# Performance work log

Measured on AMD Instinct MI355X. Metric: run time of the kernel, lower is better.

The kernel has to match this reference:

```python
import jax, jax.numpy as jnp
import numpy as np

B, S, D = 2, 2048, 1024
H, DH, DM = 16, 64, 4096
EPS = 1e-5
IGNORE = -100000.0


def setup_inputs() -> dict:
    key = jax.random.key(0)
    ks = jax.random.split(key, 14)
    s = 0.02
    return {
        "x": jax.random.normal(ks[0], (B, S, D), jnp.float32),
        "W_Q": jax.random.normal(ks[1], (H, DH, D), jnp.float32) * s,
        "W_K": jax.random.normal(ks[2], (H, DH, D), jnp.float32) * s,
        "W_V": jax.random.normal(ks[3], (H, DH, D), jnp.float32) * s,
        "W_O": jax.random.normal(ks[4], (H, D, DH), jnp.float32) * s,
        "b_Q": jax.random.normal(ks[5], (H, DH), jnp.float32) * s,
        "b_K": jax.random.normal(ks[6], (H, DH), jnp.float32) * s,
        "b_V": jax.random.normal(ks[7], (H, DH), jnp.float32) * s,
        "b_O": jax.random.normal(ks[8], (D,), jnp.float32) * s,
        "W_in": jax.random.normal(ks[9], (DM, D), jnp.float32) * s,
        "b_in": jax.random.normal(ks[10], (DM,), jnp.float32) * s,
        "W_out": jax.random.normal(ks[11], (D, DM), jnp.float32) * s,
        "b_out": jax.random.normal(ks[12], (D,), jnp.float32) * s,
    }


def ln_pre(x):
    x = x - jnp.mean(x, axis=-1, keepdims=True)
    scale = jnp.sqrt(jnp.mean(x * x, axis=-1, keepdims=True) + EPS)
    return x / scale


def gelu_new(x):
    c = np.sqrt(2.0 / np.pi).astype(np.float32)
    return 0.5 * x * (1.0 + jnp.tanh(c * (x + 0.044715 * x ** 3)))


def reference(x, W_Q, W_K, W_V, W_O, b_Q, b_K, b_V, b_O, W_in, b_in, W_out, b_out):
    resid_pre = x
    xn = ln_pre(resid_pre)
    # q,k,v: [B, S, H, DH]
    q = jnp.einsum('ihm,bpm->bpih', W_Q, xn) + b_Q
    k = jnp.einsum('ihm,bpm->bpih', W_K, xn) + b_K
    v = jnp.einsum('ihm,bpm->bpih', W_V, xn) + b_V
    attn_scale = np.sqrt(DH).astype(np.float32)
    # scores: [B, H, Sq, Sk]  (einsum 'bpih,bqih->bipq')
    scores = jnp.einsum('bpih,bqih->bipq', q, k) / attn_scale
    mask = jnp.tril(jnp.ones((S, S), bool))
    scores = jnp.where(mask, scores, IGNORE)
    attn = jax.nn.softmax(scores, axis=-1)
    # z: [B, Sq, H, DH]
    z = jnp.einsum('bpih,biqp->bqih', v, attn)
    attn_out = jnp.einsum('idh,bqih->bqd', W_O, z) + b_O
    resid_mid = resid_pre + attn_out
    m = ln_pre(resid_mid)
    pre = jnp.einsum('md,bpd->bpm', W_in, m) + b_in
    post = gelu_new(pre)
    mlp_out = jnp.einsum('dm,bpm->bpd', W_out, post) + b_out
    return resid_mid + mlp_out
```

## Files before the change

### kernel.cpp

```cpp
#include <hip/hip_runtime.h>

typedef unsigned short u16;
typedef __attribute__((ext_vector_type(8))) short short8;
typedef __attribute__((ext_vector_type(4))) unsigned short ushort4v;
typedef __attribute__((ext_vector_type(4))) float float4v;

__device__ __forceinline__ float bf2f(u16 u) {
  union { unsigned int i; float f; } c; c.i = ((unsigned int)u) << 16; return c.f;
}
__device__ __forceinline__ u16 f2bf(float f) {
  union { float f; unsigned int i; } c; c.f = f;
  unsigned int u = c.i;
  return (u16)((u + 0x7fffu + ((u >> 16) & 1u)) >> 16);
}
__device__ __forceinline__ float gelu_new(float x) {
  const float k1 = 2.30218776f;
  const float k3 = 0.10294233f;
  float x3 = x * x * x;
  float e = __builtin_amdgcn_exp2f(-(k1 * x + k3 * x3));
  return x / (1.0f + e);
}
__device__ __forceinline__ float ldres(const float* p) { return *p; }
__device__ __forceinline__ float ldres(const u16* p) { return bf2f(*p); }

__device__ __forceinline__ void gload_lds16(const u16* g, u16* l) {
  __builtin_amdgcn_global_load_lds(
      (const __attribute__((address_space(1))) unsigned int*)g,
      (__attribute__((address_space(3))) unsigned int*)l, 16, 0, 0);
}

__global__ void cvt_bf16(const float* __restrict__ src, u16* __restrict__ dst) {
  int t = blockIdx.x * 256 + threadIdx.x;
  float4v a = *(const float4v*)(src + (size_t)t * 8);
  float4v b = *(const float4v*)(src + (size_t)t * 8 + 4);
  short8 o;
#pragma unroll
  for (int j = 0; j < 4; ++j) o[j] = (short)f2bf(a[j]);
#pragma unroll
  for (int j = 0; j < 4; ++j) o[4 + j] = (short)f2bf(b[j]);
  *(short8*)(dst + (size_t)t * 8) = o;
}

__global__ void prep_wo(const float* __restrict__ WO, u16* __restrict__ Wot) {
  int t = blockIdx.x * 256 + threadIdx.x;
  int i = t >> 13;
  int d = (t >> 3) & 1023;
  int h0 = (t & 7) * 8;
  const float* src = WO + (size_t)i * 65536 + d * 64 + h0;
  float4v a = *(const float4v*)(src);
  float4v b = *(const float4v*)(src + 4);
  short8 o;
#pragma unroll
  for (int j = 0; j < 4; ++j) o[j] = (short)f2bf(a[j]);
#pragma unroll
  for (int j = 0; j < 4; ++j) o[4 + j] = (short)f2bf(b[j]);
  *(short8*)(Wot + (size_t)d * 1024 + i * 64 + h0) = o;
}

__global__ void prep_bqkv(const float* __restrict__ bQ, const float* __restrict__ bK,
                          const float* __restrict__ bV, float* __restrict__ bqkv) {
  int t = blockIdx.x * 256 + threadIdx.x;
  if (t < 3072)
    bqkv[t] = (t < 1024) ? bQ[t] : (t < 2048) ? bK[t - 1024] : bV[t - 2048];
}

__global__ void ln_f32(const float* __restrict__ x, u16* __restrict__ y) {
  __shared__ float red1[4];
  __shared__ float red2[4];
  int token = blockIdx.x;
  int tid = threadIdx.x;
  int w = tid >> 6;
  const float* xr = x + (size_t)token * 1024;
  float4v v = *(const float4v*)(xr + tid * 4);
  float s = v[0] + v[1] + v[2] + v[3];
#pragma unroll
  for (int m = 32; m >= 1; m >>= 1) s += __shfl_xor(s, m);
  if ((tid & 63) == 0) red1[w] = s;
  __syncthreads();
  float mean = (red1[0] + red1[1] + red1[2] + red1[3]) * (1.0f / 1024.0f);
  float ss = 0.0f;
#pragma unroll
  for (int j = 0; j < 4; ++j) { v[j] -= mean; ss += v[j] * v[j]; }
#pragma unroll
  for (int m = 32; m >= 1; m >>= 1) ss += __shfl_xor(ss, m);
  if ((tid & 63) == 0) red2[w] = ss;
  __syncthreads();
  float ms = (red2[0] + red2[1] + red2[2] + red2[3]) * (1.0f / 1024.0f);
  float inv = 1.0f / sqrtf(ms + 1e-5f);
  ushort4v o;
#pragma unroll
  for (int j = 0; j < 4; ++j) o[j] = f2bf(v[j] * inv);
  *(ushort4v*)(y + (size_t)token * 1024 + tid * 4) = o;
}

template <int BN, int BK, bool GELU, bool VSPLIT, typename TO, typename TR>
__global__ __launch_bounds__(256) void gemm_bt(
    const u16* __restrict__ A, const u16* __restrict__ Bw,
    const float* __restrict__ bias, const TR* __restrict__ resid,
    TO* __restrict__ C, u16* __restrict__ vTout, int M, int N, int K,
    int lda, int ldc) {
  constexpr int BM = 128;
  constexpr int SEGS = BK / 8;
  constexpr int FI = 4, FJ = BN / 32;
  constexpr int CA = BM * SEGS / 256;
  constexpr int CB = BN * SEGS / 256;
  __shared__ __align__(16) u16 As[BM * BK];
  __shared__ __align__(16) u16 Bs[BN * BK];
  const int tid = threadIdx.x;
  const int w = tid >> 6, lane = tid & 63;
  const int quad = lane >> 4, l16 = lane & 15;
  const int m0 = blockIdx.x * BM, n0 = blockIdx.y * BN;
  const int wm = (w >> 1) * 64, wn = (w & 1) * (BN / 2);
  float4v acc[FI][FJ] = {};
  for (int k0 = 0; k0 < K; k0 += BK) {
    __syncthreads();
#pragma unroll
    for (int t = 0; t < CA; ++t) {
      int chunk = (w * CA + t) * 64 + lane;
      int row = chunk / SEGS, seg = chunk % SEGS;
      gload_lds16(A + (size_t)(m0 + row) * lda + k0 + seg * 8,
                  As + (w * CA + t) * 512);
    }
#pragma unroll
    for (int t = 0; t < CB; ++t) {
      int chunk = (w * CB + t) * 64 + lane;
      int row = chunk / SEGS, seg = chunk % SEGS;
      gload_lds16(Bw + (size_t)(n0 + row) * K + k0 + seg * 8,
                  Bs + (w * CB + t) * 512);
    }
    __syncthreads();
#pragma unroll
    for (int kk = 0; kk < BK; kk += 32) {
      short8 a[FI], b[FJ];
#pragma unroll
      for (int fi = 0; fi < FI; ++fi)
        a[fi] = *(const short8*)(As + (wm + fi * 16 + l16) * BK + kk + quad * 8);
#pragma unroll
      for (int fj = 0; fj < FJ; ++fj)
        b[fj] = *(const short8*)(Bs + (wn + fj * 16 + l16) * BK + kk + quad * 8);
#pragma unroll
      for (int fi = 0; fi < FI; ++fi)
#pragma unroll
        for (int fj = 0; fj < FJ; ++fj)
          acc[fi][fj] = __builtin_amdgcn_mfma_f32_16x16x32_bf16(
              a[fi], b[fj], acc[fi][fj], 0, 0, 0);
    }
  }
#pragma unroll
  for (int fi = 0; fi < FI; ++fi) {
#pragma unroll
    for (int fj = 0; fj < FJ; ++fj) {
      int col = n0 + wn + fj * 16 + l16;
      float bv = bias ? bias[col] : 0.0f;
#pragma unroll
      for (int r = 0; r < 4; ++r) {
        int row = m0 + wm + fi * 16 + quad * 4 + r;
        float val = acc[fi][fj][r] + bv;
        if (resid) val += ldres(resid + (size_t)row * N + col);
        if (GELU) val = gelu_new(val);
        if (VSPLIT && col >= 2048) {
          vTout[(size_t)(col - 2048) * 4096 + row] = f2bf(val);
        } else if constexpr (sizeof(TO) == 2) {
          C[(size_t)row * ldc + col] = f2bf(val);
        } else {
          C[(size_t)row * ldc + col] = val;
        }
      }
    }
  }
}

__global__ __launch_bounds__(256) void attn_flash(u16* __restrict__ qk,
                                                  const u16* __restrict__ vT) {
  constexpr int PADK = 72;
  constexpr float C2 = 0.18033688011112042f;
  __shared__ __align__(16) u16 Ks[64 * PADK];
  __shared__ __align__(16) u16 Vt[64 * PADK];
  __shared__ __align__(16) u16 Ps[4][16 * PADK];
  const int id = blockIdx.x;
  const int qt = 31 - (id >> 5);
  const int combo = id & 31;
  const int head = combo >> 1, b = combo & 1;
  const int tid = threadIdx.x;
  const int w = tid >> 6, lane = tid & 63;
  const int quad = lane >> 4, l16 = lane & 15;
  const int q0 = qt * 64;
  const size_t tokB = (size_t)b * 2048;

  short8 aq[2];
#pragma unroll
  for (int ks = 0; ks < 2; ++ks)
    aq[ks] = *(const short8*)(qk + (tokB + q0 + w * 16 + l16) * 2048 +
                              head * 64 + ks * 32 + quad * 8);

  const u16* kbase = qk + tokB * 2048 + 1024 + head * 64;
  const u16* vbase = vT + (size_t)head * 64 * 4096 + tokB;

  float m_st[4] = {-1e30f, -1e30f, -1e30f, -1e30f};
  float l_st[4] = {0.f, 0.f, 0.f, 0.f};
  float4v o_acc[4] = {};

  for (int kt = 0; kt <= qt; ++kt) {
    const int kk0 = kt * 64;
    __syncthreads();
#pragma unroll
    for (int i = 0; i < 2; ++i) {
      int flat = tid * 2 + i;
      int row = flat >> 3, seg = flat & 7;
      *(short8*)(Ks + row * PADK + seg * 8) =
          *(const short8*)(kbase + (size_t)(kk0 + row) * 2048 + seg * 8);
      *(short8*)(Vt + row * PADK + seg * 8) =
          *(const short8*)(vbase + (size_t)row * 4096 + kk0 + seg * 8);
    }
    __syncthreads();

    float4v s[4];
#pragma unroll
    for (int fj = 0; fj < 4; ++fj) {
      float4v t = {0.f, 0.f, 0.f, 0.f};
#pragma unroll
      for (int ks = 0; ks < 2; ++ks) {
        short8 bk = *(const short8*)(Ks + (fj * 16 + l16) * PADK + ks * 32 + quad * 8);
        t = __builtin_amdgcn_mfma_f32_16x16x32_bf16(aq[ks], bk, t, 0, 0, 0);
      }
      s[fj] = t;
    }
#pragma unroll
    for (int fj = 0; fj < 4; ++fj)
#pragma unroll
      for (int r = 0; r < 4; ++r) s[fj][r] *= C2;
    if (kt == qt) {
#pragma unroll
      for (int fj = 0; fj < 4; ++fj) {
        int col = kk0 + fj * 16 + l16;
#pragma unroll
        for (int r = 0; r < 4; ++r) {
          int row = q0 + w * 16 + quad * 4 + r;
          if (col > row) s[fj][r] = -1e30f;
        }
      }
    }
    float mx[4];
#pragma unroll
    for (int r = 0; r < 4; ++r) {
      float m = s[0][r];
#pragma unroll
      for (int fj = 1; fj < 4; ++fj) m = fmaxf(m, s[fj][r]);
      m = fmaxf(m, __shfl_xor(m, 1));
      m = fmaxf(m, __shfl_xor(m, 2));
      m = fmaxf(m, __shfl_xor(m, 4));
      m = fmaxf(m, __shfl_xor(m, 8));
      mx[r] = m;
    }
    float alpha[4];
#pragma unroll
    for (int r = 0; r < 4; ++r) {
      float mnew = fmaxf(m_st[r], mx[r]);
      alpha[r] = __builtin_amdgcn_exp2f(m_st[r] - mnew);
      m_st[r] = mnew;
    }
    float rs[4] = {0.f, 0.f, 0.f, 0.f};
#pragma unroll
    for (int fj = 0; fj < 4; ++fj)
#pragma unroll
      for (int r = 0; r < 4; ++r) {
        float pv = __builtin_amdgcn_exp2f(s[fj][r] - m_st[r]);
        s[fj][r] = pv;
        rs[r] += pv;
      }
#pragma unroll
    for (int r = 0; r < 4; ++r) {
      float t = rs[r];
      t += __shfl_xor(t, 1);
      t += __shfl_xor(t, 2);
      t += __shfl_xor(t, 4);
      t += __shfl_xor(t, 8);
      l_st[r] = l_st[r] * alpha[r] + t;
    }
#pragma unroll
    for (int fj = 0; fj < 4; ++fj)
#pragma unroll
      for (int r = 0; r < 4; ++r) o_acc[fj][r] *= alpha[r];
#pragma unroll
    for (int fj = 0; fj < 4; ++fj)
#pragma unroll
      for (int r = 0; r < 4; ++r)
        Ps[w][(quad * 4 + r) * PADK + fj * 16 + l16] = f2bf(s[fj][r]);
    short8 ap[2];
#pragma unroll
    for (int ks = 0; ks < 2; ++ks)
      ap[ks] = *(const short8*)(&Ps[w][l16 * PADK + ks * 32 + quad * 8]);
#pragma unroll
    for (int fj = 0; fj < 4; ++fj)
#pragma unroll
      for (int ks = 0; ks < 2; ++ks) {
        short8 bv = *(const short8*)(Vt + (fj * 16 + l16) * PADK + ks * 32 + quad * 8);
        o_acc[fj] = __builtin_amdgcn_mfma_f32_16x16x32_bf16(ap[ks], bv, o_acc[fj], 0, 0, 0);
      }
  }
#pragma unroll
  for (int r = 0; r < 4; ++r) {
    float inv = 1.0f / l_st[r];
    int row = q0 + w * 16 + quad * 4 + r;
#pragma unroll
    for (int fj = 0; fj < 4; ++fj)
      qk[(tokB + row) * 2048 + head * 64 + fj * 16 + l16] =
          f2bf(o_acc[fj][r] * inv);
  }
}

extern "C" void kernel_launch(void* const* d_in, const int* in_sizes, int n_in,
                              void* d_out, int out_size, void* d_ws, size_t ws_size,
                              hipStream_t stream) {
  const float* x = (const float*)d_in[0];
  const float* W_Q = (const float*)d_in[1];
  const float* W_K = (const float*)d_in[2];
  const float* W_V = (const float*)d_in[3];
  const float* W_O = (const float*)d_in[4];
  const float* b_Q = (const float*)d_in[5];
  const float* b_K = (const float*)d_in[6];
  const float* b_V = (const float*)d_in[7];
  const float* b_O = (const float*)d_in[8];
  const float* W_in = (const float*)d_in[9];
  const float* b_in = (const float*)d_in[10];
  const float* W_out = (const float*)d_in[11];
  const float* b_out = (const float*)d_in[12];
  float* out = (float*)d_out;

  char* ws = (char*)d_ws;
  u16* Wqkv = (u16*)(ws);
  u16* Wot  = (u16*)(ws + 6291456);
  u16* Wib  = (u16*)(ws + 8388608);
  u16* Wob  = (u16*)(ws + 16777216);
  float* bqkv = (float*)(ws + 25165824);
  u16* xn   = (u16*)(ws + 25178112);
  u16* qk   = (u16*)(ws + 33566720);
  u16* vT   = (u16*)(ws + 50343936);
  u16* hbuf = (u16*)(ws + 33566720);
  float* rm = (float*)(ws + 67121152);

  cvt_bf16<<<512, 256, 0, stream>>>(W_Q, Wqkv);
  cvt_bf16<<<512, 256, 0, stream>>>(W_K, Wqkv + 1048576);
  cvt_bf16<<<512, 256, 0, stream>>>(W_V, Wqkv + 2097152);
  cvt_bf16<<<2048, 256, 0, stream>>>(W_in, Wib);
  cvt_bf16<<<2048, 256, 0, stream>>>(W_out, Wob);
  prep_wo<<<512, 256, 0, stream>>>(W_O, Wot);
  prep_bqkv<<<12, 256, 0, stream>>>(b_Q, b_K, b_V, bqkv);

  ln_f32<<<4096, 256, 0, stream>>>(x, xn);
  gemm_bt<128, 32, false, true, u16, float><<<dim3(32, 24), 256, 0, stream>>>(
      xn, Wqkv, bqkv, (const float*)nullptr, qk, vT, 4096, 3072, 1024, 1024, 2048);
  attn_flash<<<1024, 256, 0, stream>>>(qk, vT);
  gemm_bt<64, 64, false, false, float, float><<<dim3(32, 16), 256, 0, stream>>>(
      qk , Wot, b_O, x, rm, nullptr, 4096, 1024, 1024, 2048, 1024);
  ln_f32<<<4096, 256, 0, stream>>>(rm, xn);
  gemm_bt<128, 32, true, false, u16, float><<<dim3(32, 32), 256, 0, stream>>>(
      xn, Wib, b_in, (const float*)nullptr, hbuf, nullptr, 4096, 4096, 1024, 1024, 4096);
  gemm_bt<64, 64, false, false, float, float><<<dim3(32, 16), 256, 0, stream>>>(
      hbuf, Wob, b_out, rm, out, nullptr, 4096, 1024, 4096, 4096, 1024);
}
```

Before: 423.9 us.

## Use split-K with atomic accumulation for the W_O and W_out projections

Adds a split-K mode to the GEMM. Each z-slice computes a partial K range and atomically adds its result into a pre-zeroed fp32 output, and only slice 0 adds the bias and residual. The two N=1024 projection GEMMs switch to 128x128 tiles with 2-way and 4-way K splits. This keeps the block count up while using larger tiles. The cost is two memsets and fp32 atomic traffic, and the floating-point summation order becomes nondeterministic.

```diff
diff --git a/kernel.cpp b/kernel.cpp
--- a/kernel.cpp
+++ b/kernel.cpp
@@ -93,12 +93,12 @@
   *(ushort4v*)(y + (size_t)token * 1024 + tid * 4) = o;
 }
 
-template <int BN, int BK, bool GELU, bool VSPLIT, typename TO, typename TR>
+template <int BN, int BK, bool GELU, bool VSPLIT, bool ATOMIC, typename TO, typename TR>
 __global__ __launch_bounds__(256) void gemm_bt(
     const u16* __restrict__ A, const u16* __restrict__ Bw,
     const float* __restrict__ bias, const TR* __restrict__ resid,
     TO* __restrict__ C, u16* __restrict__ vTout, int M, int N, int K,
-    int lda, int ldc) {
+    int lda, int ldc, int kPer) {
   constexpr int BM = 128;
   constexpr int SEGS = BK / 8;
   constexpr int FI = 4, FJ = BN / 32;
@@ -111,8 +111,9 @@
   const int quad = lane >> 4, l16 = lane & 15;
   const int m0 = blockIdx.x * BM, n0 = blockIdx.y * BN;
   const int wm = (w >> 1) * 64, wn = (w & 1) * (BN / 2);
+  const int kBase = ATOMIC ? blockIdx.z * kPer : 0;
   float4v acc[FI][FJ] = {};
-  for (int k0 = 0; k0 < K; k0 += BK) {
+  for (int k0 = kBase; k0 < kBase + kPer; k0 += BK) {
     __syncthreads();
 #pragma unroll
     for (int t = 0; t < CA; ++t) {
@@ -146,19 +147,22 @@
               a[fi], b[fj], acc[fi][fj], 0, 0, 0);
     }
   }
+  const bool lead = !ATOMIC || blockIdx.z == 0;
 #pragma unroll
   for (int fi = 0; fi < FI; ++fi) {
 #pragma unroll
     for (int fj = 0; fj < FJ; ++fj) {
       int col = n0 + wn + fj * 16 + l16;
-      float bv = bias ? bias[col] : 0.0f;
+      float bv = (bias && lead) ? bias[col] : 0.0f;
 #pragma unroll
       for (int r = 0; r < 4; ++r) {
         int row = m0 + wm + fi * 16 + quad * 4 + r;
         float val = acc[fi][fj][r] + bv;
-        if (resid) val += ldres(resid + (size_t)row * N + col);
+        if (resid && lead) val += ldres(resid + (size_t)row * N + col);
         if (GELU) val = gelu_new(val);
-        if (VSPLIT && col >= 2048) {
+        if constexpr (ATOMIC) {
+          unsafeAtomicAdd((float*)(C + (size_t)row * ldc + col), val);
+        } else if (VSPLIT && col >= 2048) {
           vTout[(size_t)(col - 2048) * 4096 + row] = f2bf(val);
         } else if constexpr (sizeof(TO) == 2) {
           C[(size_t)row * ldc + col] = f2bf(val);
@@ -339,6 +343,9 @@
   u16* hbuf = (u16*)(ws + 33566720);
   float* rm = (float*)(ws + 67121152);
 
+  hipMemsetAsync(rm, 0, (size_t)4096 * 1024 * 4, stream);
+  hipMemsetAsync(out, 0, (size_t)4096 * 1024 * 4, stream);
+
   cvt_bf16<<<512, 256, 0, stream>>>(W_Q, Wqkv);
   cvt_bf16<<<512, 256, 0, stream>>>(W_K, Wqkv + 1048576);
   cvt_bf16<<<512, 256, 0, stream>>>(W_V, Wqkv + 2097152);
@@ -348,14 +355,14 @@
   prep_bqkv<<<12, 256, 0, stream>>>(b_Q, b_K, b_V, bqkv);
 
   ln_f32<<<4096, 256, 0, stream>>>(x, xn);
-  gemm_bt<128, 32, false, true, u16, float><<<dim3(32, 24), 256, 0, stream>>>(
-      xn, Wqkv, bqkv, (const float*)nullptr, qk, vT, 4096, 3072, 1024, 1024, 2048);
+  gemm_bt<128, 32, false, true, false, u16, float><<<dim3(32, 24), 256, 0, stream>>>(
+      xn, Wqkv, bqkv, (const float*)nullptr, qk, vT, 4096, 3072, 1024, 1024, 2048, 1024);
   attn_flash<<<1024, 256, 0, stream>>>(qk, vT);
-  gemm_bt<64, 64, false, false, float, float><<<dim3(32, 16), 256, 0, stream>>>(
-      qk , Wot, b_O, x, rm, nullptr, 4096, 1024, 1024, 2048, 1024);
+  gemm_bt<128, 32, false, false, true, float, float><<<dim3(32, 8, 2), 256, 0, stream>>>(
+      qk , Wot, b_O, x, rm, nullptr, 4096, 1024, 1024, 2048, 1024, 512);
   ln_f32<<<4096, 256, 0, stream>>>(rm, xn);
-  gemm_bt<128, 32, true, false, u16, float><<<dim3(32, 32), 256, 0, stream>>>(
-      xn, Wib, b_in, (const float*)nullptr, hbuf, nullptr, 4096, 4096, 1024, 1024, 4096);
-  gemm_bt<64, 64, false, false, float, float><<<dim3(32, 16), 256, 0, stream>>>(
-      hbuf, Wob, b_out, rm, out, nullptr, 4096, 1024, 4096, 4096, 1024);
-}
+  gemm_bt<128, 32, true, false, false, u16, float><<<dim3(32, 32), 256, 0, stream>>>(
+      xn, Wib, b_in, (const float*)nullptr, hbuf, nullptr, 4096, 4096, 1024, 1024, 4096, 1024);
+  gemm_bt<128, 32, false, false, true, float, float><<<dim3(32, 8, 4), 256, 0, stream>>>(
+      hbuf, Wob, b_out, rm, out, nullptr, 4096, 1024, 4096, 4096, 1024, 1024);
+}
```

New measurement: 471.1 us. 11.2% more time.

## Add XOR-swizzled LDS layout, double buffering, and larger K tiles to GEMM

Applied to the files above, without the earlier changes.

The GEMM kernel now XOR-swizzles 16-byte segments within each LDS row. Fragment reads for the MFMA then avoid bank conflicts. An optional double-buffered path is added and enabled for the two N=1024 GEMMs; it prefetches the next K tile while computing the current one, using one barrier per iteration instead of two. The QKV and MLP-in GEMMs switch from BK=32 to BK=64, which halves the loop iterations. Double buffering doubles LDS use and may reduce occupancy.

```diff
diff --git a/kernel.cpp b/kernel.cpp
--- a/kernel.cpp
+++ b/kernel.cpp
@@ -93,7 +93,7 @@
   *(ushort4v*)(y + (size_t)token * 1024 + tid * 4) = o;
 }
 
-template <int BN, int BK, bool GELU, bool VSPLIT, typename TO, typename TR>
+template <int BN, int BK, bool GELU, bool VSPLIT, bool DBUF, typename TO, typename TR>
 __global__ __launch_bounds__(256) void gemm_bt(
     const u16* __restrict__ A, const u16* __restrict__ Bw,
     const float* __restrict__ bias, const TR* __restrict__ resid,
@@ -101,43 +101,51 @@
     int lda, int ldc) {
   constexpr int BM = 128;
   constexpr int SEGS = BK / 8;
+  constexpr int SMASK = SEGS - 1;
   constexpr int FI = 4, FJ = BN / 32;
   constexpr int CA = BM * SEGS / 256;
   constexpr int CB = BN * SEGS / 256;
-  __shared__ __align__(16) u16 As[BM * BK];
-  __shared__ __align__(16) u16 Bs[BN * BK];
+  constexpr int NB = DBUF ? 2 : 1;
+  __shared__ __align__(16) u16 As[NB][BM * BK];
+  __shared__ __align__(16) u16 Bs[NB][BN * BK];
   const int tid = threadIdx.x;
   const int w = tid >> 6, lane = tid & 63;
   const int quad = lane >> 4, l16 = lane & 15;
   const int m0 = blockIdx.x * BM, n0 = blockIdx.y * BN;
   const int wm = (w >> 1) * 64, wn = (w & 1) * (BN / 2);
+  const int rmask = l16 & SMASK;
   float4v acc[FI][FJ] = {};
-  for (int k0 = 0; k0 < K; k0 += BK) {
-    __syncthreads();
+
+  auto stage = [&](int buf, int k0) {
 #pragma unroll
     for (int t = 0; t < CA; ++t) {
       int chunk = (w * CA + t) * 64 + lane;
       int row = chunk / SEGS, seg = chunk % SEGS;
-      gload_lds16(A + (size_t)(m0 + row) * lda + k0 + seg * 8,
-                  As + (w * CA + t) * 512);
+      int sseg = seg ^ (row & SMASK);
+      gload_lds16(A + (size_t)(m0 + row) * lda + k0 + sseg * 8,
+                  As[buf] + (w * CA + t) * 512);
     }
 #pragma unroll
     for (int t = 0; t < CB; ++t) {
       int chunk = (w * CB + t) * 64 + lane;
       int row = chunk / SEGS, seg = chunk % SEGS;
-      gload_lds16(Bw + (size_t)(n0 + row) * K + k0 + seg * 8,
-                  Bs + (w * CB + t) * 512);
-    }
-    __syncthreads();
+      int sseg = seg ^ (row & SMASK);
+      gload_lds16(Bw + (size_t)(n0 + row) * K + k0 + sseg * 8,
+                  Bs[buf] + (w * CB + t) * 512);
+    }
+  };
+  auto compute = [&](int buf) {
 #pragma unroll
     for (int kk = 0; kk < BK; kk += 32) {
       short8 a[FI], b[FJ];
 #pragma unroll
       for (int fi = 0; fi < FI; ++fi)
-        a[fi] = *(const short8*)(As + (wm + fi * 16 + l16) * BK + kk + quad * 8);
+        a[fi] = *(const short8*)(As[buf] + (wm + fi * 16 + l16) * BK +
+                                 ((((kk >> 3) + quad) ^ rmask) << 3));
 #pragma unroll
       for (int fj = 0; fj < FJ; ++fj)
-        b[fj] = *(const short8*)(Bs + (wn + fj * 16 + l16) * BK + kk + quad * 8);
+        b[fj] = *(const short8*)(Bs[buf] + (wn + fj * 16 + l16) * BK +
+                                 ((((kk >> 3) + quad) ^ rmask) << 3));
 #pragma unroll
       for (int fi = 0; fi < FI; ++fi)
 #pragma unroll
@@ -145,7 +153,27 @@
           acc[fi][fj] = __builtin_amdgcn_mfma_f32_16x16x32_bf16(
               a[fi], b[fj], acc[fi][fj], 0, 0, 0);
     }
+  };
+
+  if constexpr (DBUF) {
+    stage(0, 0);
+    __syncthreads();
+    int cur = 0;
+    for (int k0 = 0; k0 < K; k0 += BK) {
+      if (k0 + BK < K) stage(cur ^ 1, k0 + BK);
+      compute(cur);
+      __syncthreads();
+      cur ^= 1;
+    }
+  } else {
+    for (int k0 = 0; k0 < K; k0 += BK) {
+      __syncthreads();
+      stage(0, k0);
+      __syncthreads();
+      compute(0);
+    }
   }
+
 #pragma unroll
   for (int fi = 0; fi < FI; ++fi) {
 #pragma unroll
@@ -348,14 +376,14 @@
   prep_bqkv<<<12, 256, 0, stream>>>(b_Q, b_K, b_V, bqkv);
 
   ln_f32<<<4096, 256, 0, stream>>>(x, xn);
-  gemm_bt<128, 32, false, true, u16, float><<<dim3(32, 24), 256, 0, stream>>>(
+  gemm_bt<128, 64, false, true, false, u16, float><<<dim3(32, 24), 256, 0, stream>>>(
       xn, Wqkv, bqkv, (const float*)nullptr, qk, vT, 4096, 3072, 1024, 1024, 2048);
   attn_flash<<<1024, 256, 0, stream>>>(qk, vT);
-  gemm_bt<64, 64, false, false, float, float><<<dim3(32, 16), 256, 0, stream>>>(
+  gemm_bt<64, 64, false, false, true, float, float><<<dim3(32, 16), 256, 0, stream>>>(
       qk , Wot, b_O, x, rm, nullptr, 4096, 1024, 1024, 2048, 1024);
   ln_f32<<<4096, 256, 0, stream>>>(rm, xn);
-  gemm_bt<128, 32, true, false, u16, float><<<dim3(32, 32), 256, 0, stream>>>(
+  gemm_bt<128, 64, true, false, false, u16, float><<<dim3(32, 32), 256, 0, stream>>>(
       xn, Wib, b_in, (const float*)nullptr, hbuf, nullptr, 4096, 4096, 1024, 1024, 4096);
-  gemm_bt<64, 64, false, false, float, float><<<dim3(32, 16), 256, 0, stream>>>(
+  gemm_bt<64, 64, false, false, true, float, float><<<dim3(32, 16), 256, 0, stream>>>(
       hbuf, Wob, b_out, rm, out, nullptr, 4096, 1024, 4096, 4096, 1024);
 }
```

Result: faster. 406.5 us (-4.1%).
